# Performance work log

Measured on AMD Instinct MI355X. Metric: run time of the kernel, lower is better.

The kernel has to match this reference:

```python
import jax, jax.numpy as jnp
import numpy as np

N, D, N_CLASSES = 8192, 512, 128
POS_MARGIN = 1.0  # default path: sample_method=None, Dynamic_margin=None


def setup_inputs() -> dict:
    key = jax.random.key(0)
    k1, k2 = jax.random.split(key)
    x = jax.random.normal(k1, (N, D), dtype=jnp.float32)
    # metric-learning embeddings are L2-normalized so sim in [-1, 1]
    x = x / jnp.linalg.norm(x, axis=1, keepdims=True)
    targets = jax.random.randint(k2, (N,), 0, N_CLASSES, dtype=jnp.int64)
    return {"inputs": x, "targets": targets, "nonorm": 0}


def reference(inputs, targets, nonorm):
    n = inputs.shape[0]
    sim = jnp.matmul(inputs, inputs.T)                      # [n, n]
    same = targets[:, None] == targets[None, :]             # [n, n]
    pos_mask = same & (sim < POS_MARGIN)                    # drops self-sim == 1
    neg_mask = ~same

    # per-row masked log-sum-exp (sort in original is irrelevant to the sums)
    pos_sum = jnp.sum(jnp.where(pos_mask, jnp.exp(1.0 - sim), 0.0), axis=1)
    neg_sum = jnp.sum(jnp.where(neg_mask, jnp.exp(sim), 0.0), axis=1)
    pos_loss = jnp.log(pos_sum)
    neg_loss = jnp.log(neg_sum)

    has_neg = jnp.any(neg_mask, axis=1)                     # rows w/o negs are skipped
    loss = jnp.sum(jnp.where(has_neg, pos_loss + neg_loss, 0.0)) / n
    prec = jnp.mean(1.0 - has_neg.astype(jnp.float32))      # fraction of skipped rows

    # torch code reports means of the LAST row's pos/neg pairs
    last_pos = pos_mask[-1]
    last_neg = neg_mask[-1]
    mean_pos_sim = jnp.sum(jnp.where(last_pos, sim[-1], 0.0)) / jnp.sum(last_pos)
    mean_neg_sim = jnp.sum(jnp.where(last_neg, sim[-1], 0.0)) / jnp.sum(last_neg)
    return loss, prec, mean_pos_sim, mean_neg_sim
```

## Files before the change

### kernel.cpp

```cpp
#include <hip/hip_runtime.h>
#include <math.h>

#define N_ 8192
#define D_ 512
#define NC_ 128
#define T_ 64
#define BK_ 64
#define KSTEPS 8

typedef __attribute__((ext_vector_type(8))) short bf16x8;
typedef __attribute__((ext_vector_type(4))) float f32x4;
typedef __attribute__((ext_vector_type(4))) unsigned short us4;

static __device__ __forceinline__ unsigned short f2bf(float f) {
    union { float f; unsigned u; } c; c.f = f;
    unsigned u = c.u;
    u += 0x7fffu + ((u >> 16) & 1u);
    return (unsigned short)(u >> 16);
}

__global__ __launch_bounds__(256) void k_pre(const float* __restrict__ x,
                                             unsigned short* __restrict__ xb,
                                             double* __restrict__ gd,
                                             int* __restrict__ gi) {
    const int bid = blockIdx.x;
    const int tid = threadIdx.x;
    if (bid == 0 && tid == 0) {
        atomicExch((unsigned long long*)&gd[0], 0ull);
        atomicExch((unsigned long long*)&gd[1], 0ull);
        atomicExch((unsigned long long*)&gd[2], 0ull);
        atomicExch(&gi[0], 0); atomicExch(&gi[1], 0);
        atomicExch(&gi[2], 0); atomicExch(&gi[3], 0);
    }
    int i = bid * 256 + tid;
    float4 v = reinterpret_cast<const float4*>(x)[i];
    us4 o = { f2bf(v.x), f2bf(v.y), f2bf(v.z), f2bf(v.w) };
    reinterpret_cast<us4*>(xb)[i] = o;
}

__global__ __launch_bounds__(256, 2) void k_main(const unsigned short* __restrict__ xb,
                                                 const int* __restrict__ tg,
                                                 float* __restrict__ bufP,
                                                 float* __restrict__ bufN) {
    __shared__ alignas(16) unsigned short As[2][128 * 64];
    __shared__ alignas(16) unsigned short Bs[2][128 * 64];

    const int tid  = threadIdx.x;
    const int w    = tid >> 6;
    const int lane = tid & 63;
    const int q    = lane >> 4;
    const int l15  = lane & 15;
    const int wrow = w >> 1;
    const int wcol = w & 1;

    const int bswz = (blockIdx.x & 7) * 260 + (blockIdx.x >> 3);

    int rem = bswz;
    int it = 0;
    while (rem >= (T_ - it)) { rem -= (T_ - it); it++; }
    const int jt = it + rem;
    const int row0 = it * 128;
    const int col0 = jt * 128;

    auto stage_tile = [&](int p, int kt) {
        const int k0 = kt * BK_;
#pragma unroll
        for (int itr = 0; itr < 4; ++itr) {
            int gs = (itr * 4 + w) * 64 + lane;
            int r  = gs >> 3;
            int s  = gs & 7;
            int g  = s ^ (r & 7);
            const unsigned short* ga = xb + (size_t)(row0 + r) * D_ + k0 + g * 8;
            const unsigned short* gb = xb + (size_t)(col0 + r) * D_ + k0 + g * 8;
            __builtin_amdgcn_global_load_lds(
                (const __attribute__((address_space(1))) void*)ga,
                (__attribute__((address_space(3))) void*)(&As[p][0] + (itr * 4 + w) * 512),
                16, 0, 0);
            __builtin_amdgcn_global_load_lds(
                (const __attribute__((address_space(1))) void*)gb,
                (__attribute__((address_space(3))) void*)(&Bs[p][0] + (itr * 4 + w) * 512),
                16, 0, 0);
        }
    };

    f32x4 acc[4][4];
#pragma unroll
    for (int mi = 0; mi < 4; ++mi)
#pragma unroll
        for (int ni = 0; ni < 4; ++ni)
            acc[mi][ni] = (f32x4){0.f, 0.f, 0.f, 0.f};

    auto compute_tile = [&](int p) {
#pragma unroll
        for (int kc = 0; kc < 2; ++kc) {
            bf16x8 aF[4], bF[4];
#pragma unroll
            for (int mi = 0; mi < 4; ++mi) {
                int rA = wrow * 64 + mi * 16 + l15;
                int sl = (kc * 4 + q) ^ (rA & 7);
                aF[mi] = *reinterpret_cast<const bf16x8*>(&As[p][0] + rA * 64 + sl * 8);
            }
#pragma unroll
            for (int ni = 0; ni < 4; ++ni) {
                int rB = wcol * 64 + ni * 16 + l15;
                int sl = (kc * 4 + q) ^ (rB & 7);
                bF[ni] = *reinterpret_cast<const bf16x8*>(&Bs[p][0] + rB * 64 + sl * 8);
            }
            asm volatile("s_waitcnt lgkmcnt(0)" ::: "memory");
            __builtin_amdgcn_sched_barrier(0);
            __builtin_amdgcn_s_setprio(1);
#pragma unroll
            for (int mi = 0; mi < 4; ++mi)
#pragma unroll
                for (int ni = 0; ni < 4; ++ni)
                    acc[mi][ni] = __builtin_amdgcn_mfma_f32_16x16x32_bf16(
                        aF[mi], bF[ni], acc[mi][ni], 0, 0, 0);
            __builtin_amdgcn_s_setprio(0);
        }
    };

#define TILE(P, KS, DOSTAGE, VMN)                                         \
    do {                                                                  \
        asm volatile("s_waitcnt vmcnt(" #VMN ")" ::: "memory");           \
        __builtin_amdgcn_s_barrier();                                     \
        __builtin_amdgcn_sched_barrier(0);                                \
        compute_tile(P);                                                  \
        __builtin_amdgcn_s_barrier();                                     \
        __builtin_amdgcn_sched_barrier(0);                                \
        if (DOSTAGE) stage_tile(P, (KS) + 2);                             \
    } while (0)

    stage_tile(0, 0);
    stage_tile(1, 1);

    TILE(0, 0, 1, 8);
    TILE(1, 1, 1, 8);
    TILE(0, 2, 1, 8);
    TILE(1, 3, 1, 8);
    TILE(0, 4, 1, 8);
    TILE(1, 5, 1, 8);
    TILE(0, 6, 0, 8);
    TILE(1, 7, 0, 0);
#undef TILE

    int tC[4];
#pragma unroll
    for (int ni = 0; ni < 4; ++ni)
        tC[ni] = tg[col0 + wcol * 64 + ni * 16 + l15];

    float ps[4][4], ns[4][4];
    float cps[4], cns[4];
    int tR[4][4];
#pragma unroll
    for (int mi = 0; mi < 4; ++mi)
#pragma unroll
        for (int r = 0; r < 4; ++r) {
            ps[mi][r] = 0.f; ns[mi][r] = 0.f;
            tR[mi][r] = tg[row0 + wrow * 64 + mi * 16 + q * 4 + r];
        }
#pragma unroll
    for (int ni = 0; ni < 4; ++ni) { cps[ni] = 0.f; cns[ni] = 0.f; }

#pragma unroll
    for (int mi = 0; mi < 4; ++mi)
#pragma unroll
        for (int ni = 0; ni < 4; ++ni)
#pragma unroll
            for (int r = 0; r < 4; ++r) {
                float s = acc[mi][ni][r];
                bool same = (tR[mi][r] == tC[ni]);
                float e = __expf(same ? 1.0f - s : s);
                float pe = (same && (s < 1.0f)) ? e : 0.0f;
                float ne = same ? 0.0f : e;
                ps[mi][r] += pe; ns[mi][r] += ne;
                cps[ni]   += pe; cns[ni]   += ne;
            }

    float* scr = (float*)As;
#pragma unroll
    for (int mi = 0; mi < 4; ++mi)
#pragma unroll
        for (int r = 0; r < 4; ++r) {
            float p = ps[mi][r];
            float n = ns[mi][r];
#pragma unroll
            for (int m = 1; m < 16; m <<= 1) {
                p += __shfl_xor(p, m, 64);
                n += __shfl_xor(n, m, 64);
            }
            if (l15 == 0) {
                int rloc = wrow * 64 + mi * 16 + q * 4 + r;
                scr[wcol * 128 + rloc]       = p;
                scr[256 + wcol * 128 + rloc] = n;
            }
        }

#pragma unroll
    for (int ni = 0; ni < 4; ++ni) {
        float p = cps[ni];
        float n = cns[ni];
        p += __shfl_xor(p, 16, 64); p += __shfl_xor(p, 32, 64);
        n += __shfl_xor(n, 16, 64); n += __shfl_xor(n, 32, 64);
        if (q == 0) {
            int cloc = wcol * 64 + ni * 16 + l15;
            scr[512 + wrow * 128 + cloc] = p;
            scr[768 + wrow * 128 + cloc] = n;
        }
    }
    __syncthreads();

    if (tid < 128) {
        int r = tid;
        size_t off = ((size_t)it * T_ + jt) * 128 + r;
        bufP[off] = scr[r]       + scr[128 + r];
        bufN[off] = scr[256 + r] + scr[384 + r];
    } else if (jt != it) {
        int c = tid - 128;
        size_t off = ((size_t)jt * T_ + it) * 128 + c;
        bufP[off] = scr[512 + c] + scr[640 + c];
        bufN[off] = scr[768 + c] + scr[896 + c];
    }
}

__global__ __launch_bounds__(256) void k_post(const float* __restrict__ bufP,
                                              const float* __restrict__ bufN,
                                              const int* __restrict__ tg,
                                              const float* __restrict__ x,
                                              double* __restrict__ gd,
                                              int* __restrict__ gi,
                                              float* __restrict__ out) {
    __shared__ int lh[NC_];
    __shared__ float sv[256];
    __shared__ double Rd[256], Pd[256], Nd[256];
    __shared__ int Ri[256], Pc[256], Nc[256];
    const int t   = blockIdx.x;
    const int tid = threadIdx.x;

    if (tid < NC_) lh[tid] = 0;
    __syncthreads();
#pragma unroll
    for (int i = 0; i < 32; ++i) atomicAdd(&lh[tg[i * 256 + tid]], 1);
    __syncthreads();

    const int half = tid >> 7;
    const int r    = tid & 127;
    const float* buf  = half ? bufN : bufP;
    const float* base = buf + (size_t)t * T_ * 128 + r;
    float s = 0.f;
#pragma unroll
    for (int o = 0; o < T_; ++o) s += base[o * 128];
    sv[tid] = s;
    __syncthreads();

    double rd = 0.0; int ri = 0;
    if (tid < 128) {
        int row = t * 128 + tid;
        bool ok = lh[tg[row]] < N_;
        rd = ok ? (double)(logf(sv[tid]) + logf(sv[128 + tid])) : 0.0;
        ri = ok ? 0 : 1;
    }

    const int wv   = tid >> 6;
    const int lane = tid & 63;
    const int tlast = tg[N_ - 1];
    const float* xl = x + (size_t)(N_ - 1) * D_;
    double pd = 0.0, nd = 0.0;
    int pc = 0, nc = 0;
    for (int rep = 0; rep < 32; ++rep) {
        int row = t * 128 + rep * 4 + wv;
        const float* xj = x + (size_t)row * D_;
        double acc = 0.0;
#pragma unroll
        for (int itk = 0; itk < 8; ++itk) {
            int k = itk * 64 + lane;
            acc += (double)xl[k] * (double)xj[k];
        }
#pragma unroll
        for (int m = 32; m >= 1; m >>= 1) acc += __shfl_xor(acc, m, 64);
        if (lane == 0) {
            int tgr = tg[row];
            if (tgr == tlast) { if (acc < 1.0) { pd += acc; pc++; } }
            else              { nd += acc; nc++; }
        }
    }

    Rd[tid] = rd; Ri[tid] = ri;
    Pd[tid] = pd; Pc[tid] = pc;
    Nd[tid] = nd; Nc[tid] = nc;
    __syncthreads();
    for (int st = 128; st >= 1; st >>= 1) {
        if (tid < st) {
            Rd[tid] += Rd[tid + st]; Pd[tid] += Pd[tid + st]; Nd[tid] += Nd[tid + st];
            Ri[tid] += Ri[tid + st]; Pc[tid] += Pc[tid + st]; Nc[tid] += Nc[tid + st];
        }
        __syncthreads();
    }

    if (tid == 0) {
        atomicAdd(&gd[0], Rd[0]);
        atomicAdd(&gd[1], Pd[0]);
        atomicAdd(&gd[2], Nd[0]);
        atomicAdd(&gi[0], Ri[0]);
        atomicAdd(&gi[1], Pc[0]);
        atomicAdd(&gi[2], Nc[0]);
        __threadfence();
        int old = atomicAdd(&gi[3], 1);
        if ((old & 63) == 63) {
            double A = atomicAdd(&gd[0], 0.0);
            double B = atomicAdd(&gd[1], 0.0);
            double C = atomicAdd(&gd[2], 0.0);
            int U = atomicAdd(&gi[0], 0);
            int V = atomicAdd(&gi[1], 0);
            int Y = atomicAdd(&gi[2], 0);
            out[0] = (float)(A / (double)N_);
            out[1] = (float)U / (float)N_;
            out[2] = (float)(B / (double)V);
            out[3] = (float)(C / (double)Y);
        }
    }
}

extern "C" void kernel_launch(void* const* d_in, const int* in_sizes, int n_in,
                              void* d_out, int out_size, void* d_ws, size_t ws_size,
                              hipStream_t stream) {
    const float* x  = (const float*)d_in[0];
    const int*   tg = (const int*)d_in[1];
    char* ws = (char*)d_ws;

    unsigned short* xb = (unsigned short*)ws;
    const size_t XB = (size_t)N_ * D_ * 2;
    float*  bufP = (float*)(ws + XB);
    float*  bufN = (float*)(ws + XB + 2097152);
    double* gd   = (double*)(ws + XB + 4194304);
    int*    gi   = (int*)(ws + XB + 4194304 + 64);

    const int nblk_tri = T_ * (T_ + 1) / 2;

    hipLaunchKernelGGL(k_pre, dim3((N_ * D_) / (256 * 4)), dim3(256), 0, stream,
                       x, xb, gd, gi);
    hipLaunchKernelGGL(k_main, dim3(nblk_tri), dim3(256), 0, stream, xb, tg, bufP, bufN);
    hipLaunchKernelGGL(k_post, dim3(T_), dim3(256), 0, stream,
                       bufP, bufN, tg, x, gd, gi, (float*)d_out);
}
```

Measured before the change: 166.9 us.

## Process two tiles per block, prefetch next tile, and move side work into preprocessing

Each main-kernel block now handles two consecutive triangular tiles, 1040 blocks instead of 2080, and prefetches the first k-slices of the second tile while the epilogue of the first runs. The per-tile LDS fragment loads are issued all at once, with a partial lgkmcnt wait so the first half of the MFMAs can start before the second half's loads land. The last-row similarity dot products and the class histogram move from the single-wave-heavy post kernel into extra blocks of the preprocessing kernel. The scratch buffer now lives in its own shared array, which raises LDS use and may affect occupancy.

```diff
diff --git a/kernel.cpp b/kernel.cpp
--- a/kernel.cpp
+++ b/kernel.cpp
@@ -21,6 +21,9 @@
 
 __global__ __launch_bounds__(256) void k_pre(const float* __restrict__ x,
                                              unsigned short* __restrict__ xb,
+                                             const int* __restrict__ tg,
+                                             double* __restrict__ sim_last,
+                                             int* __restrict__ hist32,
                                              double* __restrict__ gd,
                                              int* __restrict__ gi) {
     const int bid = blockIdx.x;
@@ -32,10 +35,34 @@
         atomicExch(&gi[0], 0); atomicExch(&gi[1], 0);
         atomicExch(&gi[2], 0); atomicExch(&gi[3], 0);
     }
-    int i = bid * 256 + tid;
-    float4 v = reinterpret_cast<const float4*>(x)[i];
-    us4 o = { f2bf(v.x), f2bf(v.y), f2bf(v.z), f2bf(v.w) };
-    reinterpret_cast<us4*>(xb)[i] = o;
+    if (bid < 4096) {
+        int i = bid * 256 + tid;
+        float4 v = reinterpret_cast<const float4*>(x)[i];
+        us4 o = { f2bf(v.x), f2bf(v.y), f2bf(v.z), f2bf(v.w) };
+        reinterpret_cast<us4*>(xb)[i] = o;
+    } else if (bid < 6144) {
+        int j    = (bid - 4096) * 4 + (tid >> 6);
+        int lane = tid & 63;
+        const float* xl = x + (size_t)(N_ - 1) * D_;
+        const float* xj = x + (size_t)j * D_;
+        double acc = 0.0;
+#pragma unroll
+        for (int it = 0; it < 8; ++it) {
+            int k = it * 64 + lane;
+            acc += (double)xl[k] * (double)xj[k];
+        }
+#pragma unroll
+        for (int m = 32; m >= 1; m >>= 1) acc += __shfl_xor(acc, m, 64);
+        if (lane == 0) sim_last[j] = acc;
+    } else {
+        __shared__ int lh[NC_];
+        int b = bid - 6144;
+        if (tid < NC_) lh[tid] = 0;
+        __syncthreads();
+        atomicAdd(&lh[tg[b * 256 + tid]], 1);
+        __syncthreads();
+        if (tid < NC_) hist32[b * NC_ + tid] = lh[tid];
+    }
 }
 
 __global__ __launch_bounds__(256, 2) void k_main(const unsigned short* __restrict__ xb,
@@ -44,6 +71,7 @@
                                                  float* __restrict__ bufN) {
     __shared__ alignas(16) unsigned short As[2][128 * 64];
     __shared__ alignas(16) unsigned short Bs[2][128 * 64];
+    __shared__ float scr[1024];
 
     const int tid  = threadIdx.x;
     const int w    = tid >> 6;
@@ -53,16 +81,16 @@
     const int wrow = w >> 1;
     const int wcol = w & 1;
 
-    const int bswz = (blockIdx.x & 7) * 260 + (blockIdx.x >> 3);
-
-    int rem = bswz;
-    int it = 0;
+    const int bsw = (blockIdx.x & 7) * 130 + (blockIdx.x >> 3);
+    const int id0 = bsw * 2;
+
+    int rem = id0, it = 0;
     while (rem >= (T_ - it)) { rem -= (T_ - it); it++; }
-    const int jt = it + rem;
-    const int row0 = it * 128;
-    const int col0 = jt * 128;
-
-    auto stage_tile = [&](int p, int kt) {
+    int jt = it + rem;
+    int row0 = it * 128;
+    int col0 = jt * 128;
+
+    auto stage_tile = [&](int p, int kt, int r0, int c0) {
         const int k0 = kt * BK_;
 #pragma unroll
         for (int itr = 0; itr < 4; ++itr) {
@@ -70,8 +98,8 @@
             int r  = gs >> 3;
             int s  = gs & 7;
             int g  = s ^ (r & 7);
-            const unsigned short* ga = xb + (size_t)(row0 + r) * D_ + k0 + g * 8;
-            const unsigned short* gb = xb + (size_t)(col0 + r) * D_ + k0 + g * 8;
+            const unsigned short* ga = xb + (size_t)(r0 + r) * D_ + k0 + g * 8;
+            const unsigned short* gb = xb + (size_t)(c0 + r) * D_ + k0 + g * 8;
             __builtin_amdgcn_global_load_lds(
                 (const __attribute__((address_space(1))) void*)ga,
                 (__attribute__((address_space(3))) void*)(&As[p][0] + (itr * 4 + w) * 512),
@@ -84,39 +112,49 @@
     };
 
     f32x4 acc[4][4];
-#pragma unroll
-    for (int mi = 0; mi < 4; ++mi)
-#pragma unroll
-        for (int ni = 0; ni < 4; ++ni)
-            acc[mi][ni] = (f32x4){0.f, 0.f, 0.f, 0.f};
 
     auto compute_tile = [&](int p) {
-#pragma unroll
-        for (int kc = 0; kc < 2; ++kc) {
-            bf16x8 aF[4], bF[4];
-#pragma unroll
-            for (int mi = 0; mi < 4; ++mi) {
-                int rA = wrow * 64 + mi * 16 + l15;
-                int sl = (kc * 4 + q) ^ (rA & 7);
-                aF[mi] = *reinterpret_cast<const bf16x8*>(&As[p][0] + rA * 64 + sl * 8);
-            }
-#pragma unroll
-            for (int ni = 0; ni < 4; ++ni) {
-                int rB = wcol * 64 + ni * 16 + l15;
-                int sl = (kc * 4 + q) ^ (rB & 7);
-                bF[ni] = *reinterpret_cast<const bf16x8*>(&Bs[p][0] + rB * 64 + sl * 8);
-            }
-            asm volatile("s_waitcnt lgkmcnt(0)" ::: "memory");
-            __builtin_amdgcn_sched_barrier(0);
-            __builtin_amdgcn_s_setprio(1);
-#pragma unroll
-            for (int mi = 0; mi < 4; ++mi)
-#pragma unroll
-                for (int ni = 0; ni < 4; ++ni)
-                    acc[mi][ni] = __builtin_amdgcn_mfma_f32_16x16x32_bf16(
-                        aF[mi], bF[ni], acc[mi][ni], 0, 0, 0);
-            __builtin_amdgcn_s_setprio(0);
-        }
+        bf16x8 aF0[4], bF0[4], aF1[4], bF1[4];
+#pragma unroll
+        for (int mi = 0; mi < 4; ++mi) {
+            int rA = wrow * 64 + mi * 16 + l15;
+            aF0[mi] = *reinterpret_cast<const bf16x8*>(&As[p][0] + rA * 64 + (q ^ (rA & 7)) * 8);
+        }
+#pragma unroll
+        for (int ni = 0; ni < 4; ++ni) {
+            int rB = wcol * 64 + ni * 16 + l15;
+            bF0[ni] = *reinterpret_cast<const bf16x8*>(&Bs[p][0] + rB * 64 + (q ^ (rB & 7)) * 8);
+        }
+#pragma unroll
+        for (int mi = 0; mi < 4; ++mi) {
+            int rA = wrow * 64 + mi * 16 + l15;
+            aF1[mi] = *reinterpret_cast<const bf16x8*>(&As[p][0] + rA * 64 + ((4 + q) ^ (rA & 7)) * 8);
+        }
+#pragma unroll
+        for (int ni = 0; ni < 4; ++ni) {
+            int rB = wcol * 64 + ni * 16 + l15;
+            bF1[ni] = *reinterpret_cast<const bf16x8*>(&Bs[p][0] + rB * 64 + ((4 + q) ^ (rB & 7)) * 8);
+        }
+        asm volatile("s_waitcnt lgkmcnt(8)" ::: "memory");
+        __builtin_amdgcn_sched_barrier(0);
+        __builtin_amdgcn_s_setprio(1);
+#pragma unroll
+        for (int mi = 0; mi < 4; ++mi)
+#pragma unroll
+            for (int ni = 0; ni < 4; ++ni)
+                acc[mi][ni] = __builtin_amdgcn_mfma_f32_16x16x32_bf16(
+                    aF0[mi], bF0[ni], acc[mi][ni], 0, 0, 0);
+        __builtin_amdgcn_s_setprio(0);
+        asm volatile("s_waitcnt lgkmcnt(0)" ::: "memory");
+        __builtin_amdgcn_sched_barrier(0);
+        __builtin_amdgcn_s_setprio(1);
+#pragma unroll
+        for (int mi = 0; mi < 4; ++mi)
+#pragma unroll
+            for (int ni = 0; ni < 4; ++ni)
+                acc[mi][ni] = __builtin_amdgcn_mfma_f32_16x16x32_bf16(
+                    aF1[mi], bF1[ni], acc[mi][ni], 0, 0, 0);
+        __builtin_amdgcn_s_setprio(0);
     };
 
 #define TILE(P, KS, DOSTAGE, VMN)                                         \
@@ -127,105 +165,125 @@
         compute_tile(P);                                                  \
         __builtin_amdgcn_s_barrier();                                     \
         __builtin_amdgcn_sched_barrier(0);                                \
-        if (DOSTAGE) stage_tile(P, (KS) + 2);                             \
+        if (DOSTAGE) stage_tile(P, (KS) + 2, row0, col0);                 \
     } while (0)
 
-    stage_tile(0, 0);
-    stage_tile(1, 1);
-
-    TILE(0, 0, 1, 8);
-    TILE(1, 1, 1, 8);
-    TILE(0, 2, 1, 8);
-    TILE(1, 3, 1, 8);
-    TILE(0, 4, 1, 8);
-    TILE(1, 5, 1, 8);
-    TILE(0, 6, 0, 8);
-    TILE(1, 7, 0, 0);
+    stage_tile(0, 0, row0, col0);
+    stage_tile(1, 1, row0, col0);
+
+#pragma unroll 1
+    for (int pr = 0; pr < 2; ++pr) {
+#pragma unroll
+        for (int mi = 0; mi < 4; ++mi)
+#pragma unroll
+            for (int ni = 0; ni < 4; ++ni)
+                acc[mi][ni] = (f32x4){0.f, 0.f, 0.f, 0.f};
+
+        TILE(0, 0, 1, 8);
+        TILE(1, 1, 1, 8);
+        TILE(0, 2, 1, 8);
+        TILE(1, 3, 1, 8);
+        TILE(0, 4, 1, 8);
+        TILE(1, 5, 1, 8);
+        TILE(0, 6, 0, 8);
+        TILE(1, 7, 0, 0);
+
+        int itn = it, jtn = jt + 1;
+        if (jtn >= T_) { itn = it + 1; jtn = itn; }
+        const int row0n = itn * 128, col0n = jtn * 128;
+        if (pr == 0) stage_tile(0, 0, row0n, col0n);
+
+        int tC[4];
+#pragma unroll
+        for (int ni = 0; ni < 4; ++ni)
+            tC[ni] = tg[col0 + wcol * 64 + ni * 16 + l15];
+
+        float ps[4][4], ns[4][4];
+        float cps[4], cns[4];
+        int tR[4][4];
+#pragma unroll
+        for (int mi = 0; mi < 4; ++mi)
+#pragma unroll
+            for (int r = 0; r < 4; ++r) {
+                ps[mi][r] = 0.f; ns[mi][r] = 0.f;
+                tR[mi][r] = tg[row0 + wrow * 64 + mi * 16 + q * 4 + r];
+            }
+#pragma unroll
+        for (int ni = 0; ni < 4; ++ni) { cps[ni] = 0.f; cns[ni] = 0.f; }
+
+#pragma unroll
+        for (int mi = 0; mi < 4; ++mi)
+#pragma unroll
+            for (int ni = 0; ni < 4; ++ni)
+#pragma unroll
+                for (int r = 0; r < 4; ++r) {
+                    float s = acc[mi][ni][r];
+                    bool same = (tR[mi][r] == tC[ni]);
+                    float e = __expf(same ? 1.0f - s : s);
+                    float pe = (same && (s < 1.0f)) ? e : 0.0f;
+                    float ne = same ? 0.0f : e;
+                    ps[mi][r] += pe; ns[mi][r] += ne;
+                    cps[ni]   += pe; cns[ni]   += ne;
+                }
+
+#pragma unroll
+        for (int mi = 0; mi < 4; ++mi)
+#pragma unroll
+            for (int r = 0; r < 4; ++r) {
+                float p = ps[mi][r];
+                float n = ns[mi][r];
+#pragma unroll
+                for (int m = 1; m < 16; m <<= 1) {
+                    p += __shfl_xor(p, m, 64);
+                    n += __shfl_xor(n, m, 64);
+                }
+                if (l15 == 0) {
+                    int rloc = wrow * 64 + mi * 16 + q * 4 + r;
+                    scr[wcol * 128 + rloc]       = p;
+                    scr[256 + wcol * 128 + rloc] = n;
+                }
+            }
+
+#pragma unroll
+        for (int ni = 0; ni < 4; ++ni) {
+            float p = cps[ni];
+            float n = cns[ni];
+            p += __shfl_xor(p, 16, 64); p += __shfl_xor(p, 32, 64);
+            n += __shfl_xor(n, 16, 64); n += __shfl_xor(n, 32, 64);
+            if (q == 0) {
+                int cloc = wcol * 64 + ni * 16 + l15;
+                scr[512 + wrow * 128 + cloc] = p;
+                scr[768 + wrow * 128 + cloc] = n;
+            }
+        }
+        __syncthreads();
+
+        if (tid < 128) {
+            int r = tid;
+            size_t off = ((size_t)it * T_ + jt) * 128 + r;
+            bufP[off] = scr[r]       + scr[128 + r];
+            bufN[off] = scr[256 + r] + scr[384 + r];
+        } else if (jt != it) {
+            int c = tid - 128;
+            size_t off = ((size_t)jt * T_ + it) * 128 + c;
+            bufP[off] = scr[512 + c] + scr[640 + c];
+            bufN[off] = scr[768 + c] + scr[896 + c];
+        }
+        __syncthreads();
+
+        if (pr == 0) {
+            stage_tile(1, 1, row0n, col0n);
+            it = itn; jt = jtn; row0 = row0n; col0 = col0n;
+        }
+    }
 #undef TILE
-
-    int tC[4];
-#pragma unroll
-    for (int ni = 0; ni < 4; ++ni)
-        tC[ni] = tg[col0 + wcol * 64 + ni * 16 + l15];
-
-    float ps[4][4], ns[4][4];
-    float cps[4], cns[4];
-    int tR[4][4];
-#pragma unroll
-    for (int mi = 0; mi < 4; ++mi)
-#pragma unroll
-        for (int r = 0; r < 4; ++r) {
-            ps[mi][r] = 0.f; ns[mi][r] = 0.f;
-            tR[mi][r] = tg[row0 + wrow * 64 + mi * 16 + q * 4 + r];
-        }
-#pragma unroll
-    for (int ni = 0; ni < 4; ++ni) { cps[ni] = 0.f; cns[ni] = 0.f; }
-
-#pragma unroll
-    for (int mi = 0; mi < 4; ++mi)
-#pragma unroll
-        for (int ni = 0; ni < 4; ++ni)
-#pragma unroll
-            for (int r = 0; r < 4; ++r) {
-                float s = acc[mi][ni][r];
-                bool same = (tR[mi][r] == tC[ni]);
-                float e = __expf(same ? 1.0f - s : s);
-                float pe = (same && (s < 1.0f)) ? e : 0.0f;
-                float ne = same ? 0.0f : e;
-                ps[mi][r] += pe; ns[mi][r] += ne;
-                cps[ni]   += pe; cns[ni]   += ne;
-            }
-
-    float* scr = (float*)As;
-#pragma unroll
-    for (int mi = 0; mi < 4; ++mi)
-#pragma unroll
-        for (int r = 0; r < 4; ++r) {
-            float p = ps[mi][r];
-            float n = ns[mi][r];
-#pragma unroll
-            for (int m = 1; m < 16; m <<= 1) {
-                p += __shfl_xor(p, m, 64);
-                n += __shfl_xor(n, m, 64);
-            }
-            if (l15 == 0) {
-                int rloc = wrow * 64 + mi * 16 + q * 4 + r;
-                scr[wcol * 128 + rloc]       = p;
-                scr[256 + wcol * 128 + rloc] = n;
-            }
-        }
-
-#pragma unroll
-    for (int ni = 0; ni < 4; ++ni) {
-        float p = cps[ni];
-        float n = cns[ni];
-        p += __shfl_xor(p, 16, 64); p += __shfl_xor(p, 32, 64);
-        n += __shfl_xor(n, 16, 64); n += __shfl_xor(n, 32, 64);
-        if (q == 0) {
-            int cloc = wcol * 64 + ni * 16 + l15;
-            scr[512 + wrow * 128 + cloc] = p;
-            scr[768 + wrow * 128 + cloc] = n;
-        }
-    }
-    __syncthreads();
-
-    if (tid < 128) {
-        int r = tid;
-        size_t off = ((size_t)it * T_ + jt) * 128 + r;
-        bufP[off] = scr[r]       + scr[128 + r];
-        bufN[off] = scr[256 + r] + scr[384 + r];
-    } else if (jt != it) {
-        int c = tid - 128;
-        size_t off = ((size_t)jt * T_ + it) * 128 + c;
-        bufP[off] = scr[512 + c] + scr[640 + c];
-        bufN[off] = scr[768 + c] + scr[896 + c];
-    }
 }
 
 __global__ __launch_bounds__(256) void k_post(const float* __restrict__ bufP,
                                               const float* __restrict__ bufN,
                                               const int* __restrict__ tg,
-                                              const float* __restrict__ x,
+                                              const int* __restrict__ hist32,
+                                              const double* __restrict__ sim_last,
                                               double* __restrict__ gd,
                                               int* __restrict__ gi,
                                               float* __restrict__ out) {
@@ -236,11 +294,12 @@
     const int t   = blockIdx.x;
     const int tid = threadIdx.x;
 
-    if (tid < NC_) lh[tid] = 0;
-    __syncthreads();
-#pragma unroll
-    for (int i = 0; i < 32; ++i) atomicAdd(&lh[tg[i * 256 + tid]], 1);
-    __syncthreads();
+    if (tid < NC_) {
+        int a = 0;
+#pragma unroll
+        for (int b = 0; b < 32; ++b) a += hist32[b * NC_ + tid];
+        lh[tid] = a;
+    }
 
     const int half = tid >> 7;
     const int r    = tid & 127;
@@ -252,36 +311,17 @@
     sv[tid] = s;
     __syncthreads();
 
-    double rd = 0.0; int ri = 0;
+    double rd = 0.0, pd = 0.0, nd = 0.0;
+    int ri = 0, pc = 0, nc = 0;
     if (tid < 128) {
         int row = t * 128 + tid;
         bool ok = lh[tg[row]] < N_;
         rd = ok ? (double)(logf(sv[tid]) + logf(sv[128 + tid])) : 0.0;
         ri = ok ? 0 : 1;
-    }
-
-    const int wv   = tid >> 6;
-    const int lane = tid & 63;
-    const int tlast = tg[N_ - 1];
-    const float* xl = x + (size_t)(N_ - 1) * D_;
-    double pd = 0.0, nd = 0.0;
-    int pc = 0, nc = 0;
-    for (int rep = 0; rep < 32; ++rep) {
-        int row = t * 128 + rep * 4 + wv;
-        const float* xj = x + (size_t)row * D_;
-        double acc = 0.0;
-#pragma unroll
-        for (int itk = 0; itk < 8; ++itk) {
-            int k = itk * 64 + lane;
-            acc += (double)xl[k] * (double)xj[k];
-        }
-#pragma unroll
-        for (int m = 32; m >= 1; m >>= 1) acc += __shfl_xor(acc, m, 64);
-        if (lane == 0) {
-            int tgr = tg[row];
-            if (tgr == tlast) { if (acc < 1.0) { pd += acc; pc++; } }
-            else              { nd += acc; nc++; }
-        }
+        double sl = sim_last[row];
+        int tlast = tg[N_ - 1];
+        if (tg[row] == tlast) { if (sl < 1.0) { pd = sl; pc = 1; } }
+        else                  { nd = sl; nc = 1; }
     }
 
     Rd[tid] = rd; Ri[tid] = ri;
@@ -305,7 +345,7 @@
         atomicAdd(&gi[2], Nc[0]);
         __threadfence();
         int old = atomicAdd(&gi[3], 1);
-        if ((old & 63) == 63) {
+        if (old == 63) {
             double A = atomicAdd(&gd[0], 0.0);
             double B = atomicAdd(&gd[1], 0.0);
             double C = atomicAdd(&gd[2], 0.0);
@@ -331,14 +371,14 @@
     const size_t XB = (size_t)N_ * D_ * 2;
     float*  bufP = (float*)(ws + XB);
     float*  bufN = (float*)(ws + XB + 2097152);
-    double* gd   = (double*)(ws + XB + 4194304);
-    int*    gi   = (int*)(ws + XB + 4194304 + 64);
-
-    const int nblk_tri = T_ * (T_ + 1) / 2;
-
-    hipLaunchKernelGGL(k_pre, dim3((N_ * D_) / (256 * 4)), dim3(256), 0, stream,
-                       x, xb, gd, gi);
-    hipLaunchKernelGGL(k_main, dim3(nblk_tri), dim3(256), 0, stream, xb, tg, bufP, bufN);
+    double* sim_last = (double*)(ws + XB + 4194304);
+    int*    hist32   = (int*)(ws + XB + 4194304 + 65536);
+    double* gd   = (double*)(ws + XB + 4194304 + 65536 + 16384);
+    int*    gi   = (int*)(ws + XB + 4194304 + 65536 + 16384 + 64);
+
+    hipLaunchKernelGGL(k_pre, dim3(4096 + 2048 + 32), dim3(256), 0, stream,
+                       x, xb, tg, sim_last, hist32, gd, gi);
+    hipLaunchKernelGGL(k_main, dim3(1040), dim3(256), 0, stream, xb, tg, bufP, bufN);
     hipLaunchKernelGGL(k_post, dim3(T_), dim3(256), 0, stream,
-                       bufP, bufN, tg, x, gd, gi, (float*)d_out);
-}
+                       bufP, bufN, tg, hist32, sim_last, gd, gi, (float*)d_out);
+}
```

New measurement: 157.3 us. 5.7% less time.
